# Kernel tuning notes

Hardware: AMD Instinct MI355X
Metric: run time of the kernel (lower is better)

The kernel has to match this reference:

```python
import jax, jax.numpy as jnp
import numpy as np
from jax import lax

B, T, D, L = 64, 512, 1024, 32


def setup_inputs() -> dict:
    key = jax.random.key(0)
    k = jax.random.split(key, 8)
    x = jax.random.normal(k[0], (B, T, D), dtype=jnp.float32)
    mask = jnp.ones((B, T), dtype=bool)
    labels = jax.random.randint(k[1], (B, T), 0, L)
    W = jax.random.normal(k[2], (D, L), dtype=jnp.float32) / np.sqrt(D)
    b = jnp.zeros((L,), dtype=jnp.float32)
    transitions = jax.random.normal(k[3], (L, L), dtype=jnp.float32) * 0.1
    start_transitions = jax.random.normal(k[4], (L,), dtype=jnp.float32) * 0.1
    end_transitions = jax.random.normal(k[5], (L,), dtype=jnp.float32) * 0.1
    return {"x": x, "mask": mask, "labels": labels, "W": W, "b": b,
            "transitions": transitions, "start_transitions": start_transitions,
            "end_transitions": end_transitions}


def _log_partition(logits, mask, transitions, start_t, end_t):
    # logits: [B,T,L], mask: [B,T] bool. AllenNLP _input_likelihood.
    alpha0 = start_t[None, :] + logits[:, 0]  # [B,L]
    logits_t = jnp.swapaxes(logits, 0, 1)[1:]  # [T-1,B,L]
    mask_t = jnp.swapaxes(mask, 0, 1)[1:]      # [T-1,B]

    def step(alpha, inp):
        logit, m = inp  # [B,L], [B]
        # inner[b,i,j] = alpha[b,i] + transitions[i,j] + logit[b,j]
        inner = alpha[:, :, None] + transitions[None, :, :] + logit[:, None, :]
        new = jax.nn.logsumexp(inner, axis=1)
        return jnp.where(m[:, None], new, alpha), None

    alpha, _ = lax.scan(step, alpha0, (logits_t, mask_t))
    return jax.nn.logsumexp(alpha + end_t[None, :], axis=-1)  # [B]


def _joint_score(logits, tags, mask, transitions, start_t, end_t):
    # AllenNLP _joint_likelihood, vectorized over time.
    maskf = mask.astype(logits.dtype)
    score = start_t[tags[:, 0]]
    trans = transitions[tags[:, :-1], tags[:, 1:]]  # [B,T-1]
    score = score + jnp.sum(trans * maskf[:, 1:], axis=1)
    emit = jnp.take_along_axis(logits[:, :-1], tags[:, :-1, None], axis=2)[..., 0]
    score = score + jnp.sum(emit * maskf[:, :-1], axis=1)
    lengths = jnp.sum(mask.astype(jnp.int32), axis=1)
    last_tags = jnp.take_along_axis(tags, (lengths - 1)[:, None], axis=1)[:, 0]
    score = score + end_t[last_tags]
    last_emit = jnp.take_along_axis(logits[:, -1], last_tags[:, None], axis=1)[:, 0]
    score = score + last_emit * maskf[:, -1]
    return score  # [B]


def reference(x, mask, labels, W, b, transitions, start_transitions, end_transitions):
    logits = jnp.einsum('btd,dl->btl', x, W) + b  # Linear classifier
    probabilities = jax.nn.softmax(logits, axis=-1)
    logZ = _log_partition(logits, mask, transitions, start_transitions, end_transitions)
    gold = _joint_score(logits, labels, mask, transitions, start_transitions, end_transitions)
    log_likelihood = jnp.sum(gold - logZ)
    loss = -log_likelihood
    return probabilities, loss
```

## Files before the change

kernel.cpp:

```cpp
#include <hip/hip_runtime.h>

#define OUT_LOSS_IDX 1048576

typedef __attribute__((ext_vector_type(4)))  float f32x4;
typedef __attribute__((ext_vector_type(16))) float f32x16;
typedef __attribute__((ext_vector_type(4)))  int i32x4;
typedef __attribute__((ext_vector_type(4)))  unsigned u32x4;
typedef __attribute__((ext_vector_type(8)))  short bf16x8;

__device__ __forceinline__ unsigned short f32_to_bf16(float f) {
    unsigned u = __float_as_uint(f);
    unsigned r = (u + 0x7FFFu + ((u >> 16) & 1u)) >> 16;
    return (unsigned short)r;
}
__device__ __forceinline__ unsigned packbf(float lo, float hi) {
    return __builtin_amdgcn_perm(__float_as_uint(hi) + 0x8000u,
                                 __float_as_uint(lo) + 0x8000u, 0x07060302u);
}
__device__ __forceinline__ void make_bfrags(const float* c, int h, bf16x8& b0, bf16x8& b1) {
    unsigned d0 = packbf(c[0],  c[1]),  d1 = packbf(c[2],  c[3]);
    unsigned d2 = packbf(c[4],  c[5]),  d3 = packbf(c[6],  c[7]);
    unsigned d4 = packbf(c[8],  c[9]),  d5 = packbf(c[10], c[11]);
    unsigned d6 = packbf(c[12], c[13]), d7 = packbf(c[14], c[15]);
    unsigned x0 = (unsigned)__shfl_xor((int)d0, 32, 64);
    unsigned x1 = (unsigned)__shfl_xor((int)d1, 32, 64);
    unsigned x2 = (unsigned)__shfl_xor((int)d2, 32, 64);
    unsigned x3 = (unsigned)__shfl_xor((int)d3, 32, 64);
    unsigned x4 = (unsigned)__shfl_xor((int)d4, 32, 64);
    unsigned x5 = (unsigned)__shfl_xor((int)d5, 32, 64);
    unsigned x6 = (unsigned)__shfl_xor((int)d6, 32, 64);
    unsigned x7 = (unsigned)__shfl_xor((int)d7, 32, 64);
    u32x4 b0w = {h ? x2 : d0, h ? x3 : d1, h ? d2 : x0, h ? d3 : x1};
    u32x4 b1w = {h ? x6 : d4, h ? x7 : d5, h ? d6 : x4, h ? d7 : x5};
    b0 = __builtin_bit_cast(bf16x8, b0w);
    b1 = __builtin_bit_cast(bf16x8, b1w);
}
__device__ __forceinline__ void crf_step(float* c, const f32x4* ep, int h, int mk,
                                         bf16x8 a1, bf16x8 a2, int& esum) {
    bf16x8 b0, b1;
    make_bfrags(c, h, b0, b1);
    f32x16 zz = {};
    f32x16 acc = __builtin_amdgcn_mfma_f32_32x32x16_bf16(a1, b0, zz, 0, 0, 0);
    acc = __builtin_amdgcn_mfma_f32_32x32x16_bf16(a2, b1, acc, 0, 0, 0);
    f32x4 e0 = ep[h], e1 = ep[2 + h], e2 = ep[4 + h], e3 = ep[6 + h];
    int sb = __builtin_amdgcn_readfirstlane(__float_as_int(c[0]));
    int ee = ((sb >> 23) & 0xff) - 127;
    ee = ee < -60 ? -60 : (ee > 60 ? 60 : ee);
    float sc = __int_as_float((127 - ee) << 23);
    esum += ee;
    #pragma unroll
    for (int r = 0; r < 16; ++r) {
        float ev = (r < 4 ? e0[r & 3] : r < 8 ? e1[r & 3] : r < 12 ? e2[r & 3] : e3[r & 3]);
        float qn = acc[r] * (ev * sc);
        float qa = c[r] * sc;
        c[r] = mk ? qn : qa;
    }
}

__global__ void k0_wt(const float* __restrict__ W, unsigned short* __restrict__ Wt,
                      float* __restrict__ loss) {
    int idx = blockIdx.x * 256 + threadIdx.x;
    int k = idx >> 5, c = idx & 31;
    Wt[c * 1024 + k] = f32_to_bf16(W[idx]);
    if (idx == 0) loss[0] = 0.f;
}

__global__ __launch_bounds__(256) void k1_gemm(
    const float* __restrict__ x, const unsigned short* __restrict__ Wt,
    const float* __restrict__ bias, float* __restrict__ logits,
    float* __restrict__ probs) {
    __shared__ float sacc[3][64][9];
    const int tid = threadIdx.x;
    const int wv = tid >> 6, lane = tid & 63;
    const int m = lane & 15, quad = lane >> 4;
    const int r0 = blockIdx.x * 16;

    const float* xa = x + (size_t)(r0 + m) * 1024 + wv * 256 + quad * 8;
    const unsigned short* wb0 = Wt + (size_t)m * 1024 + wv * 256 + quad * 8;
    const unsigned short* wb1 = Wt + (size_t)(m + 16) * 1024 + wv * 256 + quad * 8;

    f32x4 acc0 = {0.f, 0.f, 0.f, 0.f};
    f32x4 acc1 = {0.f, 0.f, 0.f, 0.f};

    #pragma unroll
    for (int ks = 0; ks < 8; ++ks) {
        f32x4 a0 = *(const f32x4*)(xa + ks * 32);
        f32x4 a1 = *(const f32x4*)(xa + ks * 32 + 4);
        bf16x8 b0 = *(const bf16x8*)(wb0 + ks * 32);
        bf16x8 b1 = *(const bf16x8*)(wb1 + ks * 32);
        bf16x8 af;
        af[0] = (short)f32_to_bf16(a0[0]); af[1] = (short)f32_to_bf16(a0[1]);
        af[2] = (short)f32_to_bf16(a0[2]); af[3] = (short)f32_to_bf16(a0[3]);
        af[4] = (short)f32_to_bf16(a1[0]); af[5] = (short)f32_to_bf16(a1[1]);
        af[6] = (short)f32_to_bf16(a1[2]); af[7] = (short)f32_to_bf16(a1[3]);
        acc0 = __builtin_amdgcn_mfma_f32_16x16x32_bf16(af, b0, acc0, 0, 0, 0);
        acc1 = __builtin_amdgcn_mfma_f32_16x16x32_bf16(af, b1, acc1, 0, 0, 0);
    }
    if (wv) {
        #pragma unroll
        for (int r = 0; r < 4; ++r) {
            sacc[wv - 1][lane][r] = acc0[r];
            sacc[wv - 1][lane][4 + r] = acc1[r];
        }
    }
    __syncthreads();
    if (wv == 0) {
        #pragma unroll
        for (int r = 0; r < 4; ++r) {
            acc0[r] += sacc[0][lane][r] + sacc[1][lane][r] + sacc[2][lane][r];
            acc1[r] += sacc[0][lane][4 + r] + sacc[1][lane][4 + r] + sacc[2][lane][4 + r];
        }
        const float bc0 = bias[m], bc1 = bias[16 + m];
        #pragma unroll
        for (int r = 0; r < 4; ++r) {
            int row = r0 + quad * 4 + r;
            float l0 = acc0[r] + bc0;
            float l1 = acc1[r] + bc1;
            logits[row * 32 + m] = l0;
            logits[row * 32 + 16 + m] = l1;
            float mx = fmaxf(l0, l1);
            #pragma unroll
            for (int d = 1; d < 16; d <<= 1) mx = fmaxf(mx, __shfl_xor(mx, d, 64));
            float e0 = __expf(l0 - mx), e1 = __expf(l1 - mx);
            float s = e0 + e1;
            #pragma unroll
            for (int d = 1; d < 16; d <<= 1) s += __shfl_xor(s, d, 64);
            float inv = 1.0f / s;
            probs[row * 32 + m] = e0 * inv;
            probs[row * 32 + 16 + m] = e1 * inv;
        }
    }
}

__global__ __launch_bounds__(256, 1) void k3a_chunks(
    const float* __restrict__ logits, const int* __restrict__ mask,
    const float* __restrict__ trans, float* __restrict__ Gws,
    float* __restrict__ chunkLog) {
    __shared__ float sElt[128 * 32];
    __shared__ int smaskL[128];
    __shared__ float qb[4][32][33];

    const int tid = threadIdx.x;
    const int b = blockIdx.x >> 2, a = blockIdx.x & 3;
    const int w = tid >> 6, lane = tid & 63;
    const int h = lane >> 5, col = lane & 31;

    const float* src = logits + (size_t)b * 16384 + (128 * a + 1) * 32;
    #pragma unroll
    for (int q = 0; q < 4; ++q) {
        int slot = q * 256 + tid;
        f32x4 v = *(const f32x4*)&src[slot * 4];
        f32x4 e = {__expf(v[0]), __expf(v[1]), __expf(v[2]), __expf(v[3])};
        *(f32x4*)&sElt[slot * 4] = e;
    }
    if (tid < 128) {
        int t = 128 * a + 1 + tid;
        smaskL[tid] = (t < 512) ? mask[b * 512 + t] : 0;
    }
    __syncthreads();

    bf16x8 a1, a2;
    #pragma unroll
    for (int j = 0; j < 8; ++j) {
        a1[j] = (short)f32_to_bf16(__expf(trans[(8 * h + j) * 32 + col]));
        a2[j] = (short)f32_to_bf16(__expf(trans[(16 + 8 * h + j) * 32 + col]));
    }

    float cA[16], cB[16];
    #pragma unroll
    for (int r = 0; r < 16; ++r) {
        float iv = (((r & 3) + 8 * (r >> 2) + 4 * h) == col) ? 1.f : 0.f;
        cA[r] = iv; cB[r] = iv;
    }
    int esA = 0, esB = 0;

    for (int tl = 0; tl < 16; ++tl) {
        const int ttA = 32 * w + tl;
        const int ttB = 32 * w + 16 + tl;
        crf_step(cA, (const f32x4*)&sElt[ttA * 32], h, smaskL[ttA], a1, a2, esA);
        crf_step(cB, (const f32x4*)&sElt[ttB * 32], h, smaskL[ttB], a1, a2, esB);
    }

    #pragma unroll
    for (int r = 0; r < 16; ++r)
        qb[w][(r & 3) + 8 * (r >> 2) + 4 * h][col] = cB[r];
    __syncthreads();
    bf16x8 aP1, aP2;
    #pragma unroll
    for (int j = 0; j < 8; ++j) {
        aP1[j] = (short)f32_to_bf16(qb[w][col][8 * h + j]);
        aP2[j] = (short)f32_to_bf16(qb[w][col][16 + 8 * h + j]);
    }
    bf16x8 b0, b1;
    make_bfrags(cA, h, b0, b1);
    f32x16 zz = {};
    f32x16 P = __builtin_amdgcn_mfma_f32_32x32x16_bf16(aP1, b0, zz, 0, 0, 0);
    P = __builtin_amdgcn_mfma_f32_32x32x16_bf16(aP2, b1, P, 0, 0, 0);

    int sb = __builtin_amdgcn_readfirstlane(__float_as_int(P[0]));
    int ee = ((sb >> 23) & 0xff) - 127;
    ee = ee < -60 ? -60 : (ee > 60 ? 60 : ee);
    float sc = __int_as_float((127 - ee) << 23);

    const int cc = 4 * a + w;
    float* gw = Gws + (((size_t)(b * 16 + cc)) << 10);
    #pragma unroll
    for (int r = 0; r < 16; ++r)
        gw[((r & 3) + 8 * (r >> 2) + 4 * h) * 32 + col] = P[r] * sc;
    if (lane == 0)
        chunkLog[b * 16 + cc] = (float)(esA + esB + ee) * 0.6931471805599453f;
}

__global__ __launch_bounds__(64, 1) void k3b_combine(
    const float* __restrict__ logits, const int* __restrict__ mask,
    const int* __restrict__ labels, const float* __restrict__ trans,
    const float* __restrict__ start_t, const float* __restrict__ end_t,
    const float* __restrict__ Gws, const float* __restrict__ chunkLog,
    float* __restrict__ loss_out) {
    __shared__ __align__(16) float pbuf[2][32];
    __shared__ int smaskL[512];

    const int b = blockIdx.x, lane = threadIdx.x;
    const int j = lane & 31;
    const int base = b * 512;

    #pragma unroll
    for (int it = 0; it < 2; ++it) {
        int idx = it * 64 + lane;
        *(i32x4*)&smaskL[idx * 4] = *(const i32x4*)&mask[base + idx * 4];
    }
    const float* gbase = Gws + (((size_t)(b * 16)) << 10) + j * 32;
    f32x4 g0 = *(const f32x4*)&gbase[0],  g1 = *(const f32x4*)&gbase[4];
    f32x4 g2 = *(const f32x4*)&gbase[8],  g3 = *(const f32x4*)&gbase[12];
    f32x4 g4 = *(const f32x4*)&gbase[16], g5 = *(const f32x4*)&gbase[20];
    f32x4 g6 = *(const f32x4*)&gbase[24], g7 = *(const f32x4*)&gbase[28];

    float p = __expf(start_t[j] + logits[(size_t)b * 16384 + j]);
    float logC = 0.f;
    pbuf[0][j] = p;
    __syncthreads();

    for (int cc = 0; cc < 16; ++cc) {
        const float* gn = gbase + (((size_t)(cc + 1)) << 10);
        f32x4 n0, n1, n2, n3, n4, n5, n6, n7;
        if (cc < 15) {
            n0 = *(const f32x4*)&gn[0];  n1 = *(const f32x4*)&gn[4];
            n2 = *(const f32x4*)&gn[8];  n3 = *(const f32x4*)&gn[12];
            n4 = *(const f32x4*)&gn[16]; n5 = *(const f32x4*)&gn[20];
            n6 = *(const f32x4*)&gn[24]; n7 = *(const f32x4*)&gn[28];
        }
        const float* pb = pbuf[cc & 1];
        f32x4 p0 = *(const f32x4*)&pb[0],  p1 = *(const f32x4*)&pb[4];
        f32x4 p2 = *(const f32x4*)&pb[8],  p3 = *(const f32x4*)&pb[12];
        f32x4 p4 = *(const f32x4*)&pb[16], p5 = *(const f32x4*)&pb[20];
        f32x4 p6 = *(const f32x4*)&pb[24], p7 = *(const f32x4*)&pb[28];
        float r0 = p0[0];
        float s0 = 0.f, s1 = 0.f, s2 = 0.f, s3 = 0.f;
        s0 = fmaf(p0[0], g0[0], s0); s1 = fmaf(p0[1], g0[1], s1);
        s2 = fmaf(p0[2], g0[2], s2); s3 = fmaf(p0[3], g0[3], s3);
        s0 = fmaf(p1[0], g1[0], s0); s1 = fmaf(p1[1], g1[1], s1);
        s2 = fmaf(p1[2], g1[2], s2); s3 = fmaf(p1[3], g1[3], s3);
        s0 = fmaf(p2[0], g2[0], s0); s1 = fmaf(p2[1], g2[1], s1);
        s2 = fmaf(p2[2], g2[2], s2); s3 = fmaf(p2[3], g2[3], s3);
        s0 = fmaf(p3[0], g3[0], s0); s1 = fmaf(p3[1], g3[1], s1);
        s2 = fmaf(p3[2], g3[2], s2); s3 = fmaf(p3[3], g3[3], s3);
        s0 = fmaf(p4[0], g4[0], s0); s1 = fmaf(p4[1], g4[1], s1);
        s2 = fmaf(p4[2], g4[2], s2); s3 = fmaf(p4[3], g4[3], s3);
        s0 = fmaf(p5[0], g5[0], s0); s1 = fmaf(p5[1], g5[1], s1);
        s2 = fmaf(p5[2], g5[2], s2); s3 = fmaf(p5[3], g5[3], s3);
        s0 = fmaf(p6[0], g6[0], s0); s1 = fmaf(p6[1], g6[1], s1);
        s2 = fmaf(p6[2], g6[2], s2); s3 = fmaf(p6[3], g6[3], s3);
        s0 = fmaf(p7[0], g7[0], s0); s1 = fmaf(p7[1], g7[1], s1);
        s2 = fmaf(p7[2], g7[2], s2); s3 = fmaf(p7[3], g7[3], s3);
        float s = (s0 + s1) + (s2 + s3);
        p = s * __builtin_amdgcn_rcpf(r0);
        pbuf[(cc + 1) & 1][j] = p;
        logC += __logf(r0);
        g0 = n0; g1 = n1; g2 = n2; g3 = n3; g4 = n4; g5 = n5; g6 = n6; g7 = n7;
    }
    float clsum = 0.f;
    #pragma unroll
    for (int cc = 0; cc < 16; ++cc) clsum += chunkLog[b * 16 + cc];

    float f = logC + clsum + __logf(p) + end_t[j];
    float mx = f;
    #pragma unroll
    for (int d = 1; d < 32; d <<= 1) mx = fmaxf(mx, __shfl_xor(mx, d, 64));
    float e = __expf(f - mx), se = e;
    #pragma unroll
    for (int d = 1; d < 32; d <<= 1) se += __shfl_xor(se, d, 64);
    float logZb = mx + __logf(se);

    const int t0 = lane * 8;
    const int* lb = labels + base + t0;
    i32x4 la = *(const i32x4*)&lb[0];
    i32x4 lc = *(const i32x4*)&lb[4];
    int tg[8] = {la[0], la[1], la[2], la[3], lc[0], lc[1], lc[2], lc[3]};
    int prev = (lane == 0) ? 0 : labels[base + t0 - 1];
    float part = 0.f;
    int cnt = 0;
    #pragma unroll
    for (int r = 0; r < 8; ++r) {
        int t = t0 + r;
        int mk = smaskL[t];
        float mf = mk ? 1.f : 0.f;
        cnt += mk ? 1 : 0;
        int tag = tg[r];
        if (t > 0) part += trans[prev * 32 + tag] * mf;
        if (t < 511) part += logits[(size_t)b * 16384 + t * 32 + tag] * mf;
        prev = tag;
    }
    #pragma unroll
    for (int d = 1; d < 64; d <<= 1) {
        part += __shfl_xor(part, d, 64);
        cnt += __shfl_xor(cnt, d, 64);
    }
    if (lane == 0) {
        int len = cnt;
        int first = labels[base];
        int last = labels[base + len - 1];
        float g = part + start_t[first] + end_t[last];
        g += logits[(size_t)b * 16384 + 511 * 32 + last] * (smaskL[511] ? 1.f : 0.f);
        atomicAdd(loss_out, logZb - g);
    }
}

extern "C" void kernel_launch(void* const* d_in, const int* in_sizes, int n_in,
                              void* d_out, int out_size, void* d_ws, size_t ws_size,
                              hipStream_t stream) {
    const float* x       = (const float*)d_in[0];
    const int* mk        = (const int*)d_in[1];
    const int* labels    = (const int*)d_in[2];
    const float* W       = (const float*)d_in[3];
    const float* bias    = (const float*)d_in[4];
    const float* trans   = (const float*)d_in[5];
    const float* start_t = (const float*)d_in[6];
    const float* end_t   = (const float*)d_in[7];

    float* probs = (float*)d_out;
    float* loss  = probs + OUT_LOSS_IDX;
    float* ws = (float*)d_ws;
    float* logits = ws;
    unsigned short* Wt = (unsigned short*)(ws + 1048576);
    float* Gws = ws + 1048576 + 16384;
    float* chunkLog = Gws + 1048576;

    k0_wt<<<128, 256, 0, stream>>>(W, Wt, loss);
    k1_gemm<<<2048, 256, 0, stream>>>(x, Wt, bias, logits, probs);
    k3a_chunks<<<256, 256, 0, stream>>>(logits, mk, trans, Gws, chunkLog);
    k3b_combine<<<64, 64, 0, stream>>>(logits, mk, labels, trans, start_t, end_t,
                                       Gws, chunkLog, loss);
}
```

Baseline: 240.2 us.

## Use single-wave GEMM blocks with batched loads, removing split-K LDS reduction

The logits GEMM now runs one wave per block that covers the whole K dimension, instead of four waves splitting K and reducing partial sums through shared memory with a barrier. Loads are batched eight k-steps at a time to raise memory-level parallelism per wave. This removes the LDS reduction and the sync, at the cost of four times fewer waves and higher register use per wave. The combine kernel is renamed.

```diff
diff --git a/kernel.cpp b/kernel.cpp
--- a/kernel.cpp
+++ b/kernel.cpp
@@ -65,70 +65,63 @@
     if (idx == 0) loss[0] = 0.f;
 }
 
-__global__ __launch_bounds__(256) void k1_gemm(
+__global__ __launch_bounds__(64, 2) void k1_gemm(
     const float* __restrict__ x, const unsigned short* __restrict__ Wt,
     const float* __restrict__ bias, float* __restrict__ logits,
     float* __restrict__ probs) {
-    __shared__ float sacc[3][64][9];
-    const int tid = threadIdx.x;
-    const int wv = tid >> 6, lane = tid & 63;
+    const int lane = threadIdx.x;
     const int m = lane & 15, quad = lane >> 4;
     const int r0 = blockIdx.x * 16;
 
-    const float* xa = x + (size_t)(r0 + m) * 1024 + wv * 256 + quad * 8;
-    const unsigned short* wb0 = Wt + (size_t)m * 1024 + wv * 256 + quad * 8;
-    const unsigned short* wb1 = Wt + (size_t)(m + 16) * 1024 + wv * 256 + quad * 8;
+    const float* xa = x + (size_t)(r0 + m) * 1024 + quad * 8;
+    const unsigned short* wb0 = Wt + (size_t)m * 1024 + quad * 8;
+    const unsigned short* wb1 = Wt + (size_t)(m + 16) * 1024 + quad * 8;
 
     f32x4 acc0 = {0.f, 0.f, 0.f, 0.f};
     f32x4 acc1 = {0.f, 0.f, 0.f, 0.f};
 
     #pragma unroll
-    for (int ks = 0; ks < 8; ++ks) {
-        f32x4 a0 = *(const f32x4*)(xa + ks * 32);
-        f32x4 a1 = *(const f32x4*)(xa + ks * 32 + 4);
-        bf16x8 b0 = *(const bf16x8*)(wb0 + ks * 32);
-        bf16x8 b1 = *(const bf16x8*)(wb1 + ks * 32);
-        bf16x8 af;
-        af[0] = (short)f32_to_bf16(a0[0]); af[1] = (short)f32_to_bf16(a0[1]);
-        af[2] = (short)f32_to_bf16(a0[2]); af[3] = (short)f32_to_bf16(a0[3]);
-        af[4] = (short)f32_to_bf16(a1[0]); af[5] = (short)f32_to_bf16(a1[1]);
-        af[6] = (short)f32_to_bf16(a1[2]); af[7] = (short)f32_to_bf16(a1[3]);
-        acc0 = __builtin_amdgcn_mfma_f32_16x16x32_bf16(af, b0, acc0, 0, 0, 0);
-        acc1 = __builtin_amdgcn_mfma_f32_16x16x32_bf16(af, b1, acc1, 0, 0, 0);
-    }
-    if (wv) {
+    for (int ss = 0; ss < 4; ++ss) {
+        f32x4 A[16];
+        bf16x8 B0[8], B1[8];
         #pragma unroll
-        for (int r = 0; r < 4; ++r) {
-            sacc[wv - 1][lane][r] = acc0[r];
-            sacc[wv - 1][lane][4 + r] = acc1[r];
+        for (int i = 0; i < 8; ++i) {
+            const int ks = ss * 8 + i;
+            A[2 * i]     = *(const f32x4*)(xa + ks * 32);
+            A[2 * i + 1] = *(const f32x4*)(xa + ks * 32 + 4);
+            B0[i] = *(const bf16x8*)(wb0 + ks * 32);
+            B1[i] = *(const bf16x8*)(wb1 + ks * 32);
         }
-    }
-    __syncthreads();
-    if (wv == 0) {
         #pragma unroll
-        for (int r = 0; r < 4; ++r) {
-            acc0[r] += sacc[0][lane][r] + sacc[1][lane][r] + sacc[2][lane][r];
-            acc1[r] += sacc[0][lane][4 + r] + sacc[1][lane][4 + r] + sacc[2][lane][4 + r];
+        for (int i = 0; i < 8; ++i) {
+            f32x4 a0 = A[2 * i], a1 = A[2 * i + 1];
+            bf16x8 af;
+            af[0] = (short)f32_to_bf16(a0[0]); af[1] = (short)f32_to_bf16(a0[1]);
+            af[2] = (short)f32_to_bf16(a0[2]); af[3] = (short)f32_to_bf16(a0[3]);
+            af[4] = (short)f32_to_bf16(a1[0]); af[5] = (short)f32_to_bf16(a1[1]);
+            af[6] = (short)f32_to_bf16(a1[2]); af[7] = (short)f32_to_bf16(a1[3]);
+            acc0 = __builtin_amdgcn_mfma_f32_16x16x32_bf16(af, B0[i], acc0, 0, 0, 0);
+            acc1 = __builtin_amdgcn_mfma_f32_16x16x32_bf16(af, B1[i], acc1, 0, 0, 0);
         }
-        const float bc0 = bias[m], bc1 = bias[16 + m];
+    }
+    const float bc0 = bias[m], bc1 = bias[16 + m];
+    #pragma unroll
+    for (int r = 0; r < 4; ++r) {
+        int row = r0 + quad * 4 + r;
+        float l0 = acc0[r] + bc0;
+        float l1 = acc1[r] + bc1;
+        logits[row * 32 + m] = l0;
+        logits[row * 32 + 16 + m] = l1;
+        float mx = fmaxf(l0, l1);
         #pragma unroll
-        for (int r = 0; r < 4; ++r) {
-            int row = r0 + quad * 4 + r;
-            float l0 = acc0[r] + bc0;
-            float l1 = acc1[r] + bc1;
-            logits[row * 32 + m] = l0;
-            logits[row * 32 + 16 + m] = l1;
-            float mx = fmaxf(l0, l1);
-            #pragma unroll
-            for (int d = 1; d < 16; d <<= 1) mx = fmaxf(mx, __shfl_xor(mx, d, 64));
-            float e0 = __expf(l0 - mx), e1 = __expf(l1 - mx);
-            float s = e0 + e1;
-            #pragma unroll
-            for (int d = 1; d < 16; d <<= 1) s += __shfl_xor(s, d, 64);
-            float inv = 1.0f / s;
-            probs[row * 32 + m] = e0 * inv;
-            probs[row * 32 + 16 + m] = e1 * inv;
-        }
+        for (int d = 1; d < 16; d <<= 1) mx = fmaxf(mx, __shfl_xor(mx, d, 64));
+        float e0 = __expf(l0 - mx), e1 = __expf(l1 - mx);
+        float s = e0 + e1;
+        #pragma unroll
+        for (int d = 1; d < 16; d <<= 1) s += __shfl_xor(s, d, 64);
+        float inv = 1.0f / s;
+        probs[row * 32 + m] = e0 * inv;
+        probs[row * 32 + 16 + m] = e1 * inv;
     }
 }
 
@@ -211,7 +204,7 @@
         chunkLog[b * 16 + cc] = (float)(esA + esB + ee) * 0.6931471805599453f;
 }
 
-__global__ __launch_bounds__(64, 1) void k3b_combine(
+__global__ __launch_bounds__(64, 1) void kB_combine(
     const float* __restrict__ logits, const int* __restrict__ mask,
     const int* __restrict__ labels, const float* __restrict__ trans,
     const float* __restrict__ start_t, const float* __restrict__ end_t,
@@ -346,8 +339,8 @@
     float* chunkLog = Gws + 1048576;
 
     k0_wt<<<128, 256, 0, stream>>>(W, Wt, loss);
-    k1_gemm<<<2048, 256, 0, stream>>>(x, Wt, bias, logits, probs);
+    k1_gemm<<<2048, 64, 0, stream>>>(x, Wt, bias, logits, probs);
     k3a_chunks<<<256, 256, 0, stream>>>(logits, mk, trans, Gws, chunkLog);
-    k3b_combine<<<64, 64, 0, stream>>>(logits, mk, labels, trans, start_t, end_t,
-                                       Gws, chunkLog, loss);
-}
+    kB_combine<<<64, 64, 0, stream>>>(logits, mk, labels, trans, start_t, end_t,
+                                      Gws, chunkLog, loss);
+}
```

Result: no change. 243.8 us (+1.5%).
